# Kernel optimization log

Measured on AMD Instinct MI355X. Metric: run time of the kernel, lower is better.

Reference implementation:

```python
import jax, jax.numpy as jnp
import numpy as np

U, NT, BATCH, CWH = 4, 8, 128, 49152
P_NOISE = 0.02  # per-user complex noise power; stddev = sqrt(p_noise/2)


def setup_inputs() -> dict:
    key = jax.random.key(0)
    kx, kw, kh, kn = jax.random.split(key, 4)
    x = jax.random.normal(kx, (U, BATCH, CWH), dtype=jnp.float32)
    W = jax.random.normal(kw, (NT, U), dtype=jnp.float32)
    W = W / jnp.linalg.norm(W, axis=0, keepdims=True)  # unit-norm beamforming columns
    H = jax.random.normal(kh, (NT, U), dtype=jnp.float32)
    P = jnp.ones((U,), dtype=jnp.float32)
    stddev = jnp.full((U,), np.sqrt(P_NOISE / 2.0), dtype=jnp.float32)
    noise = jax.random.normal(kn, (U, BATCH, CWH), dtype=jnp.float32)  # unit noise, scaled by stddev in reference
    return {"x": x, "W": W, "H": H, "P": P, "stddev": stddev, "noise": noise}


def reference(x, W, H, P, stddev, noise):
    # x: [U, B, C]; W, H: [Nt, U]; P, stddev: [U]; noise: [U, B, C]
    sqrtP = jnp.sqrt(P)
    # combined_signal[nt] = sum_u sqrt(P_u) * W[nt,u] * x[u]  -> [Nt, B, C]
    combined = jnp.einsum('u,nu,ubc->nbc', sqrtP, W, x)
    # received_u = sum_nt H[nt,u] * combined[nt] + noise_u * stddev_u  -> [U, B, C]
    received = jnp.einsum('nu,nbc->ubc', H, combined) + noise * stddev[:, None, None]
    # amp_gain_u = sqrt(P_u) * (H[:,u] @ W[:,u])
    amp = sqrtP * jnp.einsum('nu,nu->u', H, W)
    return received / amp[:, None, None]
```

## Files before the change

kernel.cpp:

```cpp
#include <hip/hip_runtime.h>

#define UU 4
#define NTT 8
#define BC 6291456
#define BC4 1572864

__global__ __launch_bounds__(256) void chn_mu_miso_kernel(
    const float* __restrict__ x,
    const float* __restrict__ W,
    const float* __restrict__ H,
    const float* __restrict__ P,
    const float* __restrict__ stddev,
    const float* __restrict__ noise,
    float* __restrict__ out)
{
    float sqrtP[UU];
#pragma unroll
    for (int v = 0; v < UU; ++v) sqrtP[v] = sqrtf(P[v]);

    float coef[UU][UU];
    float nco[UU];
#pragma unroll
    for (int u = 0; u < UU; ++u) {
        float hw = 0.0f;
#pragma unroll
        for (int n = 0; n < NTT; ++n) hw += H[n * UU + u] * W[n * UU + u];
        const float inv_amp = 1.0f / (sqrtP[u] * hw);
#pragma unroll
        for (int v = 0; v < UU; ++v) {
            float m = 0.0f;
#pragma unroll
            for (int n = 0; n < NTT; ++n) m += H[n * UU + u] * W[n * UU + v];
            coef[u][v] = m * sqrtP[v] * inv_amp;
        }
        nco[u] = stddev[u] * inv_amp;
    }

    const int i4 = blockIdx.x * blockDim.x + threadIdx.x;
    if (i4 >= BC4) return;

    const float4* __restrict__ x4 = (const float4*)x;
    const float4* __restrict__ n4 = (const float4*)noise;
    float4* __restrict__ o4 = (float4*)out;

    float4 xv[UU];
    float4 nv[UU];
#pragma unroll
    for (int v = 0; v < UU; ++v) xv[v] = x4[v * BC4 + i4];
#pragma unroll
    for (int u = 0; u < UU; ++u) nv[u] = n4[u * BC4 + i4];

#pragma unroll
    for (int u = 0; u < UU; ++u) {
        float4 acc;
        acc.x = nco[u] * nv[u].x;
        acc.y = nco[u] * nv[u].y;
        acc.z = nco[u] * nv[u].z;
        acc.w = nco[u] * nv[u].w;
#pragma unroll
        for (int v = 0; v < UU; ++v) {
            acc.x += coef[u][v] * xv[v].x;
            acc.y += coef[u][v] * xv[v].y;
            acc.z += coef[u][v] * xv[v].z;
            acc.w += coef[u][v] * xv[v].w;
        }
        o4[u * BC4 + i4] = acc;
    }
}

extern "C" void kernel_launch(void* const* d_in, const int* in_sizes, int n_in,
                              void* d_out, int out_size, void* d_ws, size_t ws_size,
                              hipStream_t stream) {
    const float* x      = (const float*)d_in[0];
    const float* W      = (const float*)d_in[1];
    const float* H      = (const float*)d_in[2];
    const float* P      = (const float*)d_in[3];
    const float* stddev = (const float*)d_in[4];
    const float* noise  = (const float*)d_in[5];
    float* out = (float*)d_out;

    const int threads = 256;
    const int blocks = (BC4 + threads - 1) / threads;
    chn_mu_miso_kernel<<<blocks, threads, 0, stream>>>(x, W, H, P, stddev, noise, out);
}
```

Baseline: 252.0 us.

## Precompute mixing coefficients in setup kernel; tile main loop with nontemporal accesses

Moves the per-thread computation of the 4x4 mixing matrix and noise coefficients into a one-thread setup kernel that writes them to workspace, so the main kernel only loads 20 floats. The main kernel now handles four float4 groups per thread and uses nontemporal loads and stores to avoid cache pollution on streaming data. This adds a second kernel launch and a dependency through workspace memory, and the tiling reduces the number of blocks in flight.

Result: faster. 237.2 us (-5.9%).

```diff
diff --git a/kernel.cpp b/kernel.cpp
--- a/kernel.cpp
+++ b/kernel.cpp
@@ -2,24 +2,22 @@
 
 #define UU 4
 #define NTT 8
-#define BC 6291456
 #define BC4 1572864
+#define THREADS 256
+#define TILE 4
+#define NBLOCKS (BC4 / (THREADS * TILE))
 
-__global__ __launch_bounds__(256) void chn_mu_miso_kernel(
-    const float* __restrict__ x,
-    const float* __restrict__ W,
-    const float* __restrict__ H,
-    const float* __restrict__ P,
-    const float* __restrict__ stddev,
-    const float* __restrict__ noise,
-    float* __restrict__ out)
+typedef float f32x4 __attribute__((ext_vector_type(4)));
+
+__global__ __launch_bounds__(64) void coef_setup(
+    const float* __restrict__ W, const float* __restrict__ H,
+    const float* __restrict__ P, const float* __restrict__ stddev,
+    float* __restrict__ cf)
 {
+    if (threadIdx.x != 0) return;
     float sqrtP[UU];
 #pragma unroll
     for (int v = 0; v < UU; ++v) sqrtP[v] = sqrtf(P[v]);
-
-    float coef[UU][UU];
-    float nco[UU];
 #pragma unroll
     for (int u = 0; u < UU; ++u) {
         float hw = 0.0f;
@@ -31,40 +29,45 @@
             float m = 0.0f;
 #pragma unroll
             for (int n = 0; n < NTT; ++n) m += H[n * UU + u] * W[n * UU + v];
-            coef[u][v] = m * sqrtP[v] * inv_amp;
+            cf[u * UU + v] = m * sqrtP[v] * inv_amp;
         }
-        nco[u] = stddev[u] * inv_amp;
+        cf[16 + u] = stddev[u] * inv_amp;
+    }
+}
+
+__global__ __launch_bounds__(THREADS) void mix_kernel(
+    const f32x4* __restrict__ x4,
+    const f32x4* __restrict__ n4,
+    const float* __restrict__ cf,
+    f32x4* __restrict__ o4)
+{
+    float c[UU][UU], nc[UU];
+#pragma unroll
+    for (int u = 0; u < UU; ++u) {
+#pragma unroll
+        for (int v = 0; v < UU; ++v) c[u][v] = cf[u * UU + v];
+        nc[u] = cf[16 + u];
     }
 
-    const int i4 = blockIdx.x * blockDim.x + threadIdx.x;
-    if (i4 >= BC4) return;
+    const int base = blockIdx.x * (THREADS * TILE) + threadIdx.x;
+#pragma unroll
+    for (int j = 0; j < TILE; ++j) {
+        const int i4 = base + j * THREADS;
 
-    const float4* __restrict__ x4 = (const float4*)x;
-    const float4* __restrict__ n4 = (const float4*)noise;
-    float4* __restrict__ o4 = (float4*)out;
-
-    float4 xv[UU];
-    float4 nv[UU];
+        f32x4 xv[UU];
 #pragma unroll
-    for (int v = 0; v < UU; ++v) xv[v] = x4[v * BC4 + i4];
-#pragma unroll
-    for (int u = 0; u < UU; ++u) nv[u] = n4[u * BC4 + i4];
+        for (int v = 0; v < UU; ++v)
+            xv[v] = __builtin_nontemporal_load(&x4[v * BC4 + i4]);
 
 #pragma unroll
-    for (int u = 0; u < UU; ++u) {
-        float4 acc;
-        acc.x = nco[u] * nv[u].x;
-        acc.y = nco[u] * nv[u].y;
-        acc.z = nco[u] * nv[u].z;
-        acc.w = nco[u] * nv[u].w;
+        for (int u = 0; u < UU; ++u) {
+            const f32x4 nv = __builtin_nontemporal_load(&n4[u * BC4 + i4]);
+            f32x4 acc = nc[u] * nv;
 #pragma unroll
-        for (int v = 0; v < UU; ++v) {
-            acc.x += coef[u][v] * xv[v].x;
-            acc.y += coef[u][v] * xv[v].y;
-            acc.z += coef[u][v] * xv[v].z;
-            acc.w += coef[u][v] * xv[v].w;
+            for (int v = 0; v < UU; ++v)
+                acc += c[u][v] * xv[v];
+            __builtin_nontemporal_store(acc, &o4[u * BC4 + i4]);
         }
-        o4[u * BC4 + i4] = acc;
     }
 }
 
@@ -78,8 +81,9 @@
     const float* stddev = (const float*)d_in[4];
     const float* noise  = (const float*)d_in[5];
     float* out = (float*)d_out;
+    float* cf  = (float*)d_ws;
 
-    const int threads = 256;
-    const int blocks = (BC4 + threads - 1) / threads;
-    chn_mu_miso_kernel<<<blocks, threads, 0, stream>>>(x, W, H, P, stddev, noise, out);
+    coef_setup<<<1, 64, 0, stream>>>(W, H, P, stddev, cf);
+    mix_kernel<<<NBLOCKS, THREADS, 0, stream>>>(
+        (const f32x4*)x, (const f32x4*)noise, cf, (f32x4*)out);
 }
```
